# Performance work log

Measured on AMD Instinct MI355X. Metric: run time of the kernel, lower is better.

Reference implementation:

```python
import jax, jax.numpy as jnp
import numpy as np

B, S, H = 2, 2048, 2048
NH, G = 16, 4
HD = H // NH  # 128


def setup_inputs() -> dict:
    key = jax.random.key(0)
    ks = jax.random.split(key, 9)
    sc = 0.02
    x = jax.random.normal(ks[0], (B, S, H), dtype=jnp.float32)
    # causal mask: 1.0 where j > i (masked), added as mask * -1e9 (matches torch code)
    causal_mask = jnp.triu(jnp.ones((S, S), dtype=jnp.float32), k=1)[None, None]
    Wq = jax.random.normal(ks[1], (H, H), dtype=jnp.float32) * sc
    bq = jnp.zeros((H,), dtype=jnp.float32)
    Wk = jax.random.normal(ks[2], (H, G * HD), dtype=jnp.float32) * sc
    bk = jnp.zeros((G * HD,), dtype=jnp.float32)
    Wv = jax.random.normal(ks[3], (H, G * HD), dtype=jnp.float32) * sc
    bv = jnp.zeros((G * HD,), dtype=jnp.float32)
    Wo = jax.random.normal(ks[4], (H, H), dtype=jnp.float32) * sc
    bo = jnp.zeros((H,), dtype=jnp.float32)
    return {"hidden_state": x, "causal_mask": causal_mask,
            "Wq": Wq, "bq": bq, "Wk": Wk, "bk": bk,
            "Wv": Wv, "bv": bv, "Wo": Wo, "bo": bo}


def reference(hidden_state, causal_mask, Wq, bq, Wk, bk, Wv, bv, Wo, bo):
    bsz, seq_len, _ = hidden_state.shape
    npg = NH // G  # query heads per KV group
    q = hidden_state @ Wq + bq                      # [B,S,H]
    k = hidden_state @ Wk + bk                      # [B,S,G*HD]
    v = hidden_state @ Wv + bv                      # [B,S,G*HD]
    # split heads; group query heads by KV group instead of repeating K/V
    q = q.reshape(bsz, seq_len, G, npg, HD).transpose(0, 2, 3, 1, 4)   # [B,G,npg,S,HD]
    k = k.reshape(bsz, seq_len, G, HD).transpose(0, 2, 1, 3)           # [B,G,S,HD]
    v = v.reshape(bsz, seq_len, G, HD).transpose(0, 2, 1, 3)           # [B,G,S,HD]
    scale = 1.0 / jnp.sqrt(jnp.float32(HD))
    scores = jnp.einsum('bgnsd,bgtd->bgnst', q, k) * scale             # [B,G,npg,S,S]
    scores = scores + causal_mask[:, :, None] * (-1e9)
    probs = jax.nn.softmax(scores, axis=-1)
    out = jnp.einsum('bgnst,bgtd->bgnsd', probs, v)                    # [B,G,npg,S,HD]
    out = out.transpose(0, 3, 1, 2, 4).reshape(bsz, seq_len, H)        # [B,S,H]
    return out @ Wo + bo
```

## Files before the change

kernel.cpp:

```cpp
#include <hip/hip_runtime.h>
#include <hip/hip_bf16.h>

#define B_   2
#define S_   2048
#define H_   2048
#define NH_  16
#define G_   4
#define HD_  128
#define NPG_ 4
#define MROWS_ (B_ * S_)
#define KVC_   (G_ * HD_)
#define NT_    (S_ / 64)
#define QSCALE_ 0.08838834764831845f

typedef __attribute__((ext_vector_type(8))) short bf16x8;
typedef __attribute__((ext_vector_type(4))) float f32x4;

__device__ __forceinline__ short f2bf_s(float f) {
    __hip_bfloat16 h = __float2bfloat16(f);
    short s; __builtin_memcpy(&s, &h, 2); return s;
}

__device__ __forceinline__ void gll16(const void* g, void* l) {
    __builtin_amdgcn_global_load_lds(
        (const __attribute__((address_space(1))) unsigned int*)g,
        (__attribute__((address_space(3))) unsigned int*)l, 16, 0, 0);
}

struct alignas(16) bf8pack { short s[8]; };
struct alignas(8)  s4pack  { short s[4]; };

__device__ __forceinline__ bf16x8 ld2x64(const short* p) {
    s4pack lo = *(const s4pack*)p;
    s4pack hi = *(const s4pack*)(p + 4);
    bf16x8 v;
    __builtin_memcpy(&v, &lo, 8);
    __builtin_memcpy((char*)&v + 8, &hi, 8);
    return v;
}

__device__ __forceinline__ void tile_transpose(
    const float* __restrict__ in, __hip_bfloat16* __restrict__ out,
    int R, int C, int bx, int by, int tid) {
    __shared__ short tile[32][33];
    int tx = tid & 31, ty0 = tid >> 5;
    #pragma unroll
    for (int i = 0; i < 32; i += 8)
        tile[ty0 + i][tx] = f2bf_s(in[(size_t)(by * 32 + ty0 + i) * C + bx * 32 + tx]);
    __syncthreads();
    #pragma unroll
    for (int i = 0; i < 32; i += 8) {
        short s = tile[tx][ty0 + i];
        __hip_bfloat16 h; __builtin_memcpy(&h, &s, 2);
        out[(size_t)(bx * 32 + ty0 + i) * R + by * 32 + tx] = h;
    }
}

__global__ __launch_bounds__(256) void prep(
    const float* __restrict__ x,  bf8pack* __restrict__ xb,
    const float* __restrict__ Wq, __hip_bfloat16* __restrict__ WqT,
    const float* __restrict__ Wk, __hip_bfloat16* __restrict__ WkT,
    const float* __restrict__ Wv, __hip_bfloat16* __restrict__ WvT,
    const float* __restrict__ Wo, __hip_bfloat16* __restrict__ WoT,
    const float* __restrict__ bq, const float* __restrict__ bk,
    const float* __restrict__ bv, float* __restrict__ bqkv) {
    const int bid = blockIdx.x, tid = threadIdx.x;
    if (bid < 4096) {
        int i = bid * 256 + tid;
        const float4* p = (const float4*)(x + (size_t)i * 8);
        float4 a = p[0], c = p[1];
        bf8pack o;
        o.s[0] = f2bf_s(a.x); o.s[1] = f2bf_s(a.y);
        o.s[2] = f2bf_s(a.z); o.s[3] = f2bf_s(a.w);
        o.s[4] = f2bf_s(c.x); o.s[5] = f2bf_s(c.y);
        o.s[6] = f2bf_s(c.z); o.s[7] = f2bf_s(c.w);
        xb[i] = o;
    } else if (bid < 8192) {
        int t = bid - 4096;
        tile_transpose(Wq, WqT, H_, H_, t & 63, t >> 6, tid);
    } else if (bid < 9216) {
        int t = bid - 8192;
        tile_transpose(Wk, WkT, H_, KVC_, t & 15, t >> 4, tid);
    } else if (bid < 10240) {
        int t = bid - 9216;
        tile_transpose(Wv, WvT, H_, KVC_, t & 15, t >> 4, tid);
    } else if (bid < 14336) {
        int t = bid - 10240;
        tile_transpose(Wo, WoT, H_, H_, t & 63, t >> 6, tid);
    } else {
        int i = (bid - 14336) * 256 + tid;
        if (i < 3072)
            bqkv[i] = (i < 2048) ? bq[i] : (i < 2560) ? bk[i - 2048] : bv[i - 2560];
    }
}

template <int BM, int NF>
__device__ __forceinline__ void gemm_core(
    const __hip_bfloat16* __restrict__ A,
    const __hip_bfloat16* __restrict__ Bt,
    const int K, const int bm, const int bn,
    short* __restrict__ As, short* __restrict__ Bs,
    f32x4 (* __restrict__ acc)[NF])
{
    constexpr int BN  = 64 * NF;
    constexpr int MH  = BM / 64;
    constexpr int AI  = BM / 64;
    constexpr int ASZ = BM * 64;
    constexpr int BSZ = BN * 64;
    const int t = threadIdx.x;
    const int lane = t & 63, wave = t >> 6;
    const int l15 = lane & 15, quad = lane >> 4;
    const int lrow = lane >> 3, lcg = lane & 7;
    const int wm = (wave >> 2) * (BM / 2);
    const int wn = (wave & 3) * (16 * NF);
    const int nt = K >> 6;

    auto stageA = [&](int ti, int b) {
        const int kt = ti << 6;
        short* Ad = As + b * ASZ;
        #pragma unroll
        for (int p = 0; p < AI; ++p) {
            const int r0 = wave * (AI * 8) + p * 8;
            const int row = r0 + lrow;
            gll16(A + (size_t)(bm + row) * K + kt + ((lcg ^ (row & 7)) << 3),
                  Ad + r0 * 64);
        }
    };
    auto stageB = [&](int ti, int b) {
        const int kt = ti << 6;
        short* Bd = Bs + b * BSZ;
        #pragma unroll
        for (int p = 0; p < NF; ++p) {
            const int r0 = wave * (NF * 8) + p * 8;
            const int row = r0 + lrow;
            gll16(Bt + (size_t)(bn + row) * K + kt + ((lcg ^ (row & 7)) << 3),
                  Bd + r0 * 64);
        }
    };

    stageA(0, 0); stageB(0, 0);
    stageA(1, 1); stageB(1, 1);

    for (int ti = 0; ti < nt; ++ti) {
        const int b = ti & 1;
        const short* Ab = As + b * ASZ;
        const short* Bb = Bs + b * BSZ;

        if (ti == nt - 1) {
            asm volatile("s_waitcnt vmcnt(0)" ::: "memory");
        } else if constexpr (AI + NF == 7) {
            asm volatile("s_waitcnt vmcnt(7)" ::: "memory");
        } else if constexpr (AI + NF == 6) {
            asm volatile("s_waitcnt vmcnt(6)" ::: "memory");
        } else {
            asm volatile("s_waitcnt vmcnt(0)" ::: "memory");
        }
        asm volatile("s_barrier" ::: "memory");

        bf16x8 bfr[NF][2], af0[MH][2], af1[MH][2];
        #pragma unroll
        for (int n = 0; n < NF; ++n) {
            const int rb = wn + n * 16 + l15;
            #pragma unroll
            for (int ks = 0; ks < 2; ++ks)
                bfr[n][ks] = *(const bf16x8*)(Bb + rb * 64 +
                    (((ks * 4 + quad) ^ (rb & 7)) << 3));
        }
        #pragma unroll
        for (int i = 0; i < MH; ++i) {
            const int ra = wm + i * 16 + l15;
            #pragma unroll
            for (int ks = 0; ks < 2; ++ks)
                af0[i][ks] = *(const bf16x8*)(Ab + ra * 64 +
                    (((ks * 4 + quad) ^ (ra & 7)) << 3));
        }
        #pragma unroll
        for (int i = 0; i < MH; ++i) {
            const int ra = wm + (MH + i) * 16 + l15;
            #pragma unroll
            for (int ks = 0; ks < 2; ++ks)
                af1[i][ks] = *(const bf16x8*)(Ab + ra * 64 +
                    (((ks * 4 + quad) ^ (ra & 7)) << 3));
        }

        __builtin_amdgcn_s_setprio(1);
        #pragma unroll
        for (int ks = 0; ks < 2; ++ks)
            #pragma unroll
            for (int i = 0; i < MH; ++i)
                #pragma unroll
                for (int n = 0; n < NF; ++n)
                    acc[i][n] = __builtin_amdgcn_mfma_f32_16x16x32_bf16(
                        af0[i][ks], bfr[n][ks], acc[i][n], 0, 0, 0);
        #pragma unroll
        for (int ks = 0; ks < 2; ++ks)
            #pragma unroll
            for (int i = 0; i < MH; ++i)
                #pragma unroll
                for (int n = 0; n < NF; ++n)
                    acc[MH + i][n] = __builtin_amdgcn_mfma_f32_16x16x32_bf16(
                        af1[i][ks], bfr[n][ks], acc[MH + i][n], 0, 0, 0);
        __builtin_amdgcn_s_setprio(0);

        asm volatile("s_barrier" ::: "memory");
        if (ti + 2 < nt) { stageA(ti + 2, b); stageB(ti + 2, b); }
    }
}

__global__ __launch_bounds__(512, 2) void gemm_qkv8(
    const __hip_bfloat16* __restrict__ A,
    const __hip_bfloat16* __restrict__ Bt,
    const float* __restrict__ bias,
    __hip_bfloat16* __restrict__ Qo,
    __hip_bfloat16* __restrict__ Ko,
    __hip_bfloat16* __restrict__ VtG) {
    __shared__ __align__(16) short As[2 * 256 * 64];
    __shared__ __align__(16) short Bs[2 * 192 * 64];
    const int bid = blockIdx.x;
    const int s = (bid & 7) * 32 + (bid >> 3);
    const int bm = (s & 15) * 256, bn = (s >> 4) * 192;

    f32x4 acc[8][3] = {};
    gemm_core<256, 3>(A, Bt, H_, bm, bn, As, Bs, acc);

    const int t = threadIdx.x;
    const int lane = t & 63, wave = t >> 6;
    const int l15 = lane & 15, quad = lane >> 4;
    const int wm = (wave >> 2) * 128, wn = (wave & 3) * 48;

    #pragma unroll
    for (int i = 0; i < 8; ++i) {
        int row0 = bm + wm + i * 16 + quad * 4;
        #pragma unroll
        for (int j = 0; j < 3; ++j) {
            int c0 = bn + wn + j * 16;
            int colg = c0 + l15;
            float bv = bias[colg];
            if (c0 < 2048) {
                #pragma unroll
                for (int r = 0; r < 4; ++r)
                    Qo[(size_t)(row0 + r) * H_ + colg] =
                        __float2bfloat16((acc[i][j][r] + bv) * QSCALE_);
            } else if (c0 < 2560) {
                #pragma unroll
                for (int r = 0; r < 4; ++r)
                    Ko[(size_t)(row0 + r) * KVC_ + (colg - 2048)] =
                        __float2bfloat16(acc[i][j][r] + bv);
            } else {
                int coll = colg - 2560;
                short s4v[4];
                #pragma unroll
                for (int r = 0; r < 4; ++r) s4v[r] = f2bf_s(acc[i][j][r] + bv);
                *(uint2*)(&VtG[(size_t)coll * MROWS_ + row0]) = *(uint2*)s4v;
            }
        }
    }
}

__global__ __launch_bounds__(512, 2) void gemm_out8(
    const __hip_bfloat16* __restrict__ A,
    const __hip_bfloat16* __restrict__ Bt,
    const float* __restrict__ bias,
    float* __restrict__ C) {
    __shared__ __align__(16) short As[2 * 128 * 64];
    __shared__ __align__(16) short Bs[2 * 256 * 64];
    const int bid = blockIdx.x;
    const int s = (bid & 7) * 32 + (bid >> 3);
    const int bm = (s & 31) * 128, bn = (s >> 5) * 256;

    f32x4 acc[4][4] = {};
    gemm_core<128, 4>(A, Bt, H_, bm, bn, As, Bs, acc);

    const int t = threadIdx.x;
    const int lane = t & 63, wave = t >> 6;
    const int l15 = lane & 15, quad = lane >> 4;
    const int wm = (wave >> 2) * 64, wn = (wave & 3) * 64;

    #pragma unroll
    for (int i = 0; i < 4; ++i) {
        int row0 = bm + wm + i * 16 + quad * 4;
        #pragma unroll
        for (int j = 0; j < 4; ++j) {
            int col = bn + wn + j * 16 + l15;
            float bv = bias[col];
            #pragma unroll
            for (int r = 0; r < 4; ++r)
                C[(size_t)(row0 + r) * H_ + col] = acc[i][j][r] + bv;
        }
    }
}

__global__ __launch_bounds__(256, 2) void attn_causal_gqa(
    const __hip_bfloat16* __restrict__ Q,
    const __hip_bfloat16* __restrict__ K,
    const __hip_bfloat16* __restrict__ VtG,
    __hip_bfloat16* __restrict__ O) {
    __shared__ short KsL[64 * 128];
    __shared__ short VtL[128 * 64];
    __shared__ short Ps[4][2][16 * 72];

    const int h  = blockIdx.x;
    const int b  = h >> 4;
    const int hh = h & 15;
    const int g  = hh >> 2;
    const int qb1 = blockIdx.y;
    const int qb2 = NT_ - 1 - qb1;

    const int t = threadIdx.x;
    const int lane = t & 63, wave = t >> 6;
    const int l15 = lane & 15, quad = lane >> 4;
    const int swz = l15 & 7;

    const __hip_bfloat16* Qb = Q + (size_t)b * S_ * H_ + hh * HD_;
    const __hip_bfloat16* Kb = K + (size_t)b * S_ * KVC_ + g * HD_;
    const __hip_bfloat16* Vg = VtG + (size_t)g * HD_ * MROWS_ + b * S_;

    bf16x8 aq1[4], aq2[4];
    {
        const int qr1 = qb1 * 64 + wave * 16 + l15;
        const int qr2 = qb2 * 64 + wave * 16 + l15;
        #pragma unroll
        for (int kk = 0; kk < 4; ++kk) {
            aq1[kk] = *(const bf16x8*)(Qb + (size_t)qr1 * H_ + kk * 32 + quad * 8);
            aq2[kk] = *(const bf16x8*)(Qb + (size_t)qr2 * H_ + kk * 32 + quad * 8);
        }
    }

    f32x4 o1[8] = {}, o2[8] = {};
    float lp1 = 0.f, lp2 = 0.f;
    const int qrow_loc = wave * 16 + l15;

    for (int tile = 0; tile <= qb2; ++tile) {
        const int key0 = tile * 64;
        const bool do1 = (tile <= qb1);

        #pragma unroll
        for (int p = 0; p < 4; ++p) {
            int R0 = wave * 16 + p * 4;
            int row = R0 + (lane >> 4);
            int cg = ((lane & 15) ^ (row & 7)) * 8;
            gll16(Kb + (size_t)(key0 + row) * KVC_ + cg, &KsL[R0 * 128]);
        }
        #pragma unroll
        for (int p = 0; p < 4; ++p) {
            int R0 = wave * 32 + p * 8;
            int row = R0 + (lane >> 3);
            int cg = ((lane & 7) ^ (row & 7)) * 8;
            gll16(Vg + (size_t)row * MROWS_ + key0 + cg, &VtL[R0 * 64]);
        }
        __syncthreads();

        f32x4 s2[4] = {}, s1[4] = {};
        #pragma unroll
        for (int kk = 0; kk < 4; ++kk) {
            bf16x8 bk[4];
            #pragma unroll
            for (int nt = 0; nt < 4; ++nt)
                bk[nt] = *(const bf16x8*)(
                    &KsL[(nt * 16 + l15) * 128 + (((kk * 4 + quad) ^ swz) * 8)]);
            #pragma unroll
            for (int nt = 0; nt < 4; ++nt)
                s2[nt] = __builtin_amdgcn_mfma_f32_16x16x32_bf16(
                    bk[nt], aq2[kk], s2[nt], 0, 0, 0);
            if (do1) {
                #pragma unroll
                for (int nt = 0; nt < 4; ++nt)
                    s1[nt] = __builtin_amdgcn_mfma_f32_16x16x32_bf16(
                        bk[nt], aq1[kk], s1[nt], 0, 0, 0);
            }
        }

        __asm__ volatile("" ::: "memory");
        short* P2 = &Ps[wave][1][0];
        {
            const bool m2 = (tile == qb2);
            #pragma unroll
            for (int nt = 0; nt < 4; ++nt) {
                s4pack pk;
                #pragma unroll
                for (int r = 0; r < 4; ++r) {
                    float p = __expf(s2[nt][r]);
                    if (m2 && (nt * 16 + quad * 4 + r > qrow_loc)) p = 0.f;
                    lp2 += p;
                    pk.s[r] = f2bf_s(p);
                }
                *(s4pack*)&P2[l15 * 72 + nt * 16 + quad * 4] = pk;
            }
        }
        short* P1 = &Ps[wave][0][0];
        if (do1) {
            const bool m1 = (tile == qb1);
            #pragma unroll
            for (int nt = 0; nt < 4; ++nt) {
                s4pack pk;
                #pragma unroll
                for (int r = 0; r < 4; ++r) {
                    float p = __expf(s1[nt][r]);
                    if (m1 && (nt * 16 + quad * 4 + r > qrow_loc)) p = 0.f;
                    lp1 += p;
                    pk.s[r] = f2bf_s(p);
                }
                *(s4pack*)&P1[l15 * 72 + nt * 16 + quad * 4] = pk;
            }
        }
        __asm__ volatile("" ::: "memory");

        #pragma unroll
        for (int ks = 0; ks < 2; ++ks) {
            bf16x8 ap2 = ld2x64(&P2[l15 * 72 + ks * 32 + quad * 8]);
            bf16x8 ap1;
            if (do1) ap1 = ld2x64(&P1[l15 * 72 + ks * 32 + quad * 8]);
            #pragma unroll
            for (int n2 = 0; n2 < 8; ++n2) {
                bf16x8 bv = *(const bf16x8*)(
                    &VtL[(n2 * 16 + l15) * 64 + (((ks * 4 + quad) ^ swz) * 8)]);
                o2[n2] = __builtin_amdgcn_mfma_f32_16x16x32_bf16(
                    ap2, bv, o2[n2], 0, 0, 0);
                if (do1)
                    o1[n2] = __builtin_amdgcn_mfma_f32_16x16x32_bf16(
                        ap1, bv, o1[n2], 0, 0, 0);
            }
        }
        __syncthreads();
    }

    float L1 = lp1, L2 = lp2;
    L1 += __shfl_xor(L1, 16); L2 += __shfl_xor(L2, 16);
    L1 += __shfl_xor(L1, 32); L2 += __shfl_xor(L2, 32);
    #pragma unroll
    for (int r = 0; r < 4; ++r) {
        float i1 = 1.f / __shfl(L1, quad * 4 + r);
        float i2 = 1.f / __shfl(L2, quad * 4 + r);
        int s1r = qb1 * 64 + wave * 16 + quad * 4 + r;
        int s2r = qb2 * 64 + wave * 16 + quad * 4 + r;
        #pragma unroll
        for (int n2 = 0; n2 < 8; ++n2) {
            int d = n2 * 16 + l15;
            O[((size_t)b * S_ + s1r) * H_ + hh * HD_ + d] = __float2bfloat16(o1[n2][r] * i1);
            O[((size_t)b * S_ + s2r) * H_ + hh * HD_ + d] = __float2bfloat16(o2[n2][r] * i2);
        }
    }
}

extern "C" void kernel_launch(void* const* d_in, const int* in_sizes, int n_in,
                              void* d_out, int out_size, void* d_ws, size_t ws_size,
                              hipStream_t stream) {
    const float* x  = (const float*)d_in[0];
    const float* Wq = (const float*)d_in[2];
    const float* bq = (const float*)d_in[3];
    const float* Wk = (const float*)d_in[4];
    const float* bk = (const float*)d_in[5];
    const float* Wv = (const float*)d_in[6];
    const float* bv = (const float*)d_in[7];
    const float* Wo = (const float*)d_in[8];
    const float* bo = (const float*)d_in[9];
    float* out = (float*)d_out;

    char* ws = (char*)d_ws;
    const size_t MB = 1024 * 1024;
    __hip_bfloat16* xb   = (__hip_bfloat16*)(ws);
    __hip_bfloat16* WT   = (__hip_bfloat16*)(ws + 16 * MB);
    __hip_bfloat16* Kws  = (__hip_bfloat16*)(ws + 28 * MB);
    __hip_bfloat16* VtG  = (__hip_bfloat16*)(ws + 32 * MB);
    __hip_bfloat16* WoT  = (__hip_bfloat16*)(ws + 36 * MB);
    float*          bqkv = (float*)         (ws + 44 * MB);
    __hip_bfloat16* Aws  = (__hip_bfloat16*)(ws);
    __hip_bfloat16* Qbuf = (__hip_bfloat16*)d_out;

    prep<<<14348, 256, 0, stream>>>(
        x, (bf8pack*)xb,
        Wq, WT,
        Wk, WT + (size_t)2048 * H_,
        Wv, WT + (size_t)2560 * H_,
        Wo, WoT,
        bq, bk, bv, bqkv);

    gemm_qkv8<<<256, 512, 0, stream>>>(xb, WT, bqkv, Qbuf, Kws, VtG);

    attn_causal_gqa<<<dim3(B_ * NH_, NT_ / 2), 256, 0, stream>>>(Qbuf, Kws, VtG, Aws);

    gemm_out8<<<256, 512, 0, stream>>>(Aws, WoT, bo, out);
}
```

Baseline: 302.5 us.

## Restructure GEMM core pipelining, widen QKV tiles, and double-buffer K in attention

```diff
diff --git a/kernel.cpp b/kernel.cpp
--- a/kernel.cpp
+++ b/kernel.cpp
@@ -94,30 +94,31 @@
     }
 }
 
-template <int BM, int NF>
+template <int BM>
 __device__ __forceinline__ void gemm_core(
     const __hip_bfloat16* __restrict__ A,
     const __hip_bfloat16* __restrict__ Bt,
     const int K, const int bm, const int bn,
     short* __restrict__ As, short* __restrict__ Bs,
-    f32x4 (* __restrict__ acc)[NF])
+    f32x4 (* __restrict__ acc)[4])
 {
-    constexpr int BN  = 64 * NF;
-    constexpr int MH  = BM / 64;
+    constexpr int MF  = BM / 32;
+    constexpr int MH  = MF / 2;
     constexpr int AI  = BM / 64;
     constexpr int ASZ = BM * 64;
-    constexpr int BSZ = BN * 64;
-    const int t = threadIdx.x;
-    const int lane = t & 63, wave = t >> 6;
+    constexpr int BSZ = 256 * 64;
+    const int t0 = threadIdx.x;
+    const int lane = t0 & 63, wave = t0 >> 6;
     const int l15 = lane & 15, quad = lane >> 4;
     const int lrow = lane >> 3, lcg = lane & 7;
     const int wm = (wave >> 2) * (BM / 2);
-    const int wn = (wave & 3) * (16 * NF);
+    const int wn = (wave & 3) * 64;
     const int nt = K >> 6;
 
-    auto stageA = [&](int ti, int b) {
+    auto stage = [&](int ti) {
         const int kt = ti << 6;
-        short* Ad = As + b * ASZ;
+        short* Ad = As + (ti & 1) * ASZ;
+        short* Bd = Bs + (ti & 1) * BSZ;
         #pragma unroll
         for (int p = 0; p < AI; ++p) {
             const int r0 = wave * (AI * 8) + p * 8;
@@ -125,45 +126,30 @@
             gll16(A + (size_t)(bm + row) * K + kt + ((lcg ^ (row & 7)) << 3),
                   Ad + r0 * 64);
         }
-    };
-    auto stageB = [&](int ti, int b) {
-        const int kt = ti << 6;
-        short* Bd = Bs + b * BSZ;
-        #pragma unroll
-        for (int p = 0; p < NF; ++p) {
-            const int r0 = wave * (NF * 8) + p * 8;
+        #pragma unroll
+        for (int p = 0; p < 4; ++p) {
+            const int r0 = wave * 32 + p * 8;
             const int row = r0 + lrow;
             gll16(Bt + (size_t)(bn + row) * K + kt + ((lcg ^ (row & 7)) << 3),
                   Bd + r0 * 64);
         }
     };
 
-    stageA(0, 0); stageB(0, 0);
-    stageA(1, 1); stageB(1, 1);
-
-    for (int ti = 0; ti < nt; ++ti) {
-        const int b = ti & 1;
-        const short* Ab = As + b * ASZ;
-        const short* Bb = Bs + b * BSZ;
-
-        if (ti == nt - 1) {
-            asm volatile("s_waitcnt vmcnt(0)" ::: "memory");
-        } else if constexpr (AI + NF == 7) {
-            asm volatile("s_waitcnt vmcnt(7)" ::: "memory");
-        } else if constexpr (AI + NF == 6) {
-            asm volatile("s_waitcnt vmcnt(6)" ::: "memory");
-        } else {
-            asm volatile("s_waitcnt vmcnt(0)" ::: "memory");
-        }
-        asm volatile("s_barrier" ::: "memory");
-
-        bf16x8 bfr[NF][2], af0[MH][2], af1[MH][2];
-        #pragma unroll
-        for (int n = 0; n < NF; ++n) {
+    stage(0);
+    asm volatile("s_waitcnt vmcnt(0)" ::: "memory");
+    asm volatile("s_barrier" ::: "memory");
+
+    for (int t = 0; t < nt; ++t) {
+        const short* Ab = As + (t & 1) * ASZ;
+        const short* Bb = Bs + (t & 1) * BSZ;
+        bf16x8 b01[2][2], b23[2][2], ah[MH][2];
+
+        #pragma unroll
+        for (int n = 0; n < 2; ++n) {
             const int rb = wn + n * 16 + l15;
             #pragma unroll
             for (int ks = 0; ks < 2; ++ks)
-                bfr[n][ks] = *(const bf16x8*)(Bb + rb * 64 +
+                b01[n][ks] = *(const bf16x8*)(Bb + rb * 64 +
                     (((ks * 4 + quad) ^ (rb & 7)) << 3));
         }
         #pragma unroll
@@ -171,39 +157,80 @@
             const int ra = wm + i * 16 + l15;
             #pragma unroll
             for (int ks = 0; ks < 2; ++ks)
-                af0[i][ks] = *(const bf16x8*)(Ab + ra * 64 +
+                ah[i][ks] = *(const bf16x8*)(Ab + ra * 64 +
                     (((ks * 4 + quad) ^ (ra & 7)) << 3));
         }
+        if (t + 1 < nt) stage(t + 1);
+        asm volatile("s_barrier" ::: "memory");
+        asm volatile("s_waitcnt lgkmcnt(0)" ::: "memory");
+        __builtin_amdgcn_s_setprio(1);
+        #pragma unroll
+        for (int ks = 0; ks < 2; ++ks)
+            #pragma unroll
+            for (int i = 0; i < MH; ++i)
+                #pragma unroll
+                for (int n = 0; n < 2; ++n)
+                    acc[i][n] = __builtin_amdgcn_mfma_f32_16x16x32_bf16(
+                        ah[i][ks], b01[n][ks], acc[i][n], 0, 0, 0);
+        __builtin_amdgcn_s_setprio(0);
+        asm volatile("s_barrier" ::: "memory");
+
+        #pragma unroll
+        for (int n = 0; n < 2; ++n) {
+            const int rb = wn + (2 + n) * 16 + l15;
+            #pragma unroll
+            for (int ks = 0; ks < 2; ++ks)
+                b23[n][ks] = *(const bf16x8*)(Bb + rb * 64 +
+                    (((ks * 4 + quad) ^ (rb & 7)) << 3));
+        }
+        asm volatile("s_barrier" ::: "memory");
+        asm volatile("s_waitcnt lgkmcnt(0)" ::: "memory");
+        __builtin_amdgcn_s_setprio(1);
+        #pragma unroll
+        for (int ks = 0; ks < 2; ++ks)
+            #pragma unroll
+            for (int i = 0; i < MH; ++i)
+                #pragma unroll
+                for (int n = 0; n < 2; ++n)
+                    acc[i][2 + n] = __builtin_amdgcn_mfma_f32_16x16x32_bf16(
+                        ah[i][ks], b23[n][ks], acc[i][2 + n], 0, 0, 0);
+        __builtin_amdgcn_s_setprio(0);
+        asm volatile("s_barrier" ::: "memory");
+
         #pragma unroll
         for (int i = 0; i < MH; ++i) {
             const int ra = wm + (MH + i) * 16 + l15;
             #pragma unroll
             for (int ks = 0; ks < 2; ++ks)
-                af1[i][ks] = *(const bf16x8*)(Ab + ra * 64 +
+                ah[i][ks] = *(const bf16x8*)(Ab + ra * 64 +
                     (((ks * 4 + quad) ^ (ra & 7)) << 3));
         }
-
+        asm volatile("s_barrier" ::: "memory");
+        asm volatile("s_waitcnt lgkmcnt(0)" ::: "memory");
         __builtin_amdgcn_s_setprio(1);
         #pragma unroll
         for (int ks = 0; ks < 2; ++ks)
             #pragma unroll
             for (int i = 0; i < MH; ++i)
                 #pragma unroll
-                for (int n = 0; n < NF; ++n)
-                    acc[i][n] = __builtin_amdgcn_mfma_f32_16x16x32_bf16(
-                        af0[i][ks], bfr[n][ks], acc[i][n], 0, 0, 0);
+                for (int n = 0; n < 2; ++n)
+                    acc[MH + i][2 + n] = __builtin_amdgcn_mfma_f32_16x16x32_bf16(
+                        ah[i][ks], b23[n][ks], acc[MH + i][2 + n], 0, 0, 0);
+        __builtin_amdgcn_s_setprio(0);
+        asm volatile("s_barrier" ::: "memory");
+
+        __builtin_amdgcn_s_setprio(1);
         #pragma unroll
         for (int ks = 0; ks < 2; ++ks)
             #pragma unroll
             for (int i = 0; i < MH; ++i)
                 #pragma unroll
-                for (int n = 0; n < NF; ++n)
+                for (int n = 0; n < 2; ++n)
                     acc[MH + i][n] = __builtin_amdgcn_mfma_f32_16x16x32_bf16(
-                        af1[i][ks], bfr[n][ks], acc[MH + i][n], 0, 0, 0);
+                        ah[i][ks], b01[n][ks], acc[MH + i][n], 0, 0, 0);
         __builtin_amdgcn_s_setprio(0);
-
-        asm volatile("s_barrier" ::: "memory");
-        if (ti + 2 < nt) { stageA(ti + 2, b); stageB(ti + 2, b); }
+        asm volatile("s_waitcnt vmcnt(0)" ::: "memory");
+        asm volatile("s_barrier" ::: "memory");
     }
 }
 
@@ -215,24 +242,24 @@
     __hip_bfloat16* __restrict__ Ko,
     __hip_bfloat16* __restrict__ VtG) {
     __shared__ __align__(16) short As[2 * 256 * 64];
-    __shared__ __align__(16) short Bs[2 * 192 * 64];
+    __shared__ __align__(16) short Bs[2 * 256 * 64];
     const int bid = blockIdx.x;
-    const int s = (bid & 7) * 32 + (bid >> 3);
-    const int bm = (s & 15) * 256, bn = (s >> 4) * 192;
-
-    f32x4 acc[8][3] = {};
-    gemm_core<256, 3>(A, Bt, H_, bm, bn, As, Bs, acc);
+    const int s = (bid & 7) * 24 + (bid >> 3);
+    const int bm = (s & 15) * 256, bn = (s >> 4) * 256;
+
+    f32x4 acc[8][4] = {};
+    gemm_core<256>(A, Bt, H_, bm, bn, As, Bs, acc);
 
     const int t = threadIdx.x;
     const int lane = t & 63, wave = t >> 6;
     const int l15 = lane & 15, quad = lane >> 4;
-    const int wm = (wave >> 2) * 128, wn = (wave & 3) * 48;
+    const int wm = (wave >> 2) * 128, wn = (wave & 3) * 64;
 
     #pragma unroll
     for (int i = 0; i < 8; ++i) {
         int row0 = bm + wm + i * 16 + quad * 4;
         #pragma unroll
-        for (int j = 0; j < 3; ++j) {
+        for (int j = 0; j < 4; ++j) {
             int c0 = bn + wn + j * 16;
             int colg = c0 + l15;
             float bv = bias[colg];
@@ -269,7 +296,7 @@
     const int bm = (s & 31) * 128, bn = (s >> 5) * 256;
 
     f32x4 acc[4][4] = {};
-    gemm_core<128, 4>(A, Bt, H_, bm, bn, As, Bs, acc);
+    gemm_core<128>(A, Bt, H_, bm, bn, As, Bs, acc);
 
     const int t = threadIdx.x;
     const int lane = t & 63, wave = t >> 6;
@@ -295,9 +322,9 @@
     const __hip_bfloat16* __restrict__ K,
     const __hip_bfloat16* __restrict__ VtG,
     __hip_bfloat16* __restrict__ O) {
-    __shared__ short KsL[64 * 128];
+    __shared__ short KsL[2][64 * 128];
     __shared__ short VtL[128 * 64];
-    __shared__ short Ps[4][2][16 * 72];
+    __shared__ short Ps[4][2][16 * 76];
 
     const int h  = blockIdx.x;
     const int b  = h >> 4;
@@ -315,6 +342,26 @@
     const __hip_bfloat16* Kb = K + (size_t)b * S_ * KVC_ + g * HD_;
     const __hip_bfloat16* Vg = VtG + (size_t)g * HD_ * MROWS_ + b * S_;
 
+    auto stageK = [&](int tile) {
+        short* kd = &KsL[tile & 1][0];
+        #pragma unroll
+        for (int p = 0; p < 4; ++p) {
+            int R0 = wave * 16 + p * 4;
+            int row = R0 + (lane >> 4);
+            int cg = ((lane & 15) ^ (row & 7)) * 8;
+            gll16(Kb + (size_t)(tile * 64 + row) * KVC_ + cg, &kd[R0 * 128]);
+        }
+    };
+    auto stageV = [&](int tile) {
+        #pragma unroll
+        for (int p = 0; p < 4; ++p) {
+            int R0 = wave * 32 + p * 8;
+            int row = R0 + (lane >> 3);
+            int cg = ((lane & 7) ^ (row & 7)) * 8;
+            gll16(Vg + (size_t)row * MROWS_ + tile * 64 + cg, &VtL[R0 * 64]);
+        }
+    };
+
     bf16x8 aq1[4], aq2[4];
     {
         const int qr1 = qb1 * 64 + wave * 16 + l15;
@@ -330,25 +377,20 @@
     float lp1 = 0.f, lp2 = 0.f;
     const int qrow_loc = wave * 16 + l15;
 
+    stageK(0);
+
     for (int tile = 0; tile <= qb2; ++tile) {
-        const int key0 = tile * 64;
         const bool do1 = (tile <= qb1);
-
-        #pragma unroll
-        for (int p = 0; p < 4; ++p) {
-            int R0 = wave * 16 + p * 4;
-            int row = R0 + (lane >> 4);
-            int cg = ((lane & 15) ^ (row & 7)) * 8;
-            gll16(Kb + (size_t)(key0 + row) * KVC_ + cg, &KsL[R0 * 128]);
-        }
-        #pragma unroll
-        for (int p = 0; p < 4; ++p) {
-            int R0 = wave * 32 + p * 8;
-            int row = R0 + (lane >> 3);
-            int cg = ((lane & 7) ^ (row & 7)) * 8;
-            gll16(Vg + (size_t)row * MROWS_ + key0 + cg, &VtL[R0 * 64]);
-        }
-        __syncthreads();
+        const bool last = (tile == qb2);
+
+        stageV(tile);
+        if (!last) stageK(tile + 1);
+
+        if (!last) asm volatile("s_waitcnt vmcnt(8)" ::: "memory");
+        else       asm volatile("s_waitcnt vmcnt(4)" ::: "memory");
+        asm volatile("s_barrier" ::: "memory");
+
+        const short* kb = &KsL[tile & 1][0];
 
         f32x4 s2[4] = {}, s1[4] = {};
         #pragma unroll
@@ -357,7 +399,7 @@
             #pragma unroll
             for (int nt = 0; nt < 4; ++nt)
                 bk[nt] = *(const bf16x8*)(
-                    &KsL[(nt * 16 + l15) * 128 + (((kk * 4 + quad) ^ swz) * 8)]);
+                    &kb[(nt * 16 + l15) * 128 + (((kk * 4 + quad) ^ swz) * 8)]);
             #pragma unroll
             for (int nt = 0; nt < 4; ++nt)
                 s2[nt] = __builtin_amdgcn_mfma_f32_16x16x32_bf16(
@@ -384,7 +426,7 @@
                     lp2 += p;
                     pk.s[r] = f2bf_s(p);
                 }
-                *(s4pack*)&P2[l15 * 72 + nt * 16 + quad * 4] = pk;
+                *(s4pack*)&P2[l15 * 76 + nt * 16 + quad * 4] = pk;
             }
         }
         short* P1 = &Ps[wave][0][0];
@@ -400,16 +442,20 @@
                     lp1 += p;
                     pk.s[r] = f2bf_s(p);
                 }
-                *(s4pack*)&P1[l15 * 72 + nt * 16 + quad * 4] = pk;
+                *(s4pack*)&P1[l15 * 76 + nt * 16 + quad * 4] = pk;
             }
         }
         __asm__ volatile("" ::: "memory");
 
+        if (!last) asm volatile("s_waitcnt vmcnt(4)" ::: "memory");
+        else       asm volatile("s_waitcnt vmcnt(0)" ::: "memory");
+        asm volatile("s_barrier" ::: "memory");
+
         #pragma unroll
         for (int ks = 0; ks < 2; ++ks) {
-            bf16x8 ap2 = ld2x64(&P2[l15 * 72 + ks * 32 + quad * 8]);
+            bf16x8 ap2 = ld2x64(&P2[l15 * 76 + ks * 32 + quad * 8]);
             bf16x8 ap1;
-            if (do1) ap1 = ld2x64(&P1[l15 * 72 + ks * 32 + quad * 8]);
+            if (do1) ap1 = ld2x64(&P1[l15 * 76 + ks * 32 + quad * 8]);
             #pragma unroll
             for (int n2 = 0; n2 < 8; ++n2) {
                 bf16x8 bv = *(const bf16x8*)(
@@ -421,7 +467,7 @@
                         ap1, bv, o1[n2], 0, 0, 0);
             }
         }
-        __syncthreads();
+        asm volatile("s_barrier" ::: "memory");
     }
 
     float L1 = lp1, L2 = lp2;
@@ -475,7 +521,7 @@
         Wo, WoT,
         bq, bk, bv, bqkv);
 
-    gemm_qkv8<<<256, 512, 0, stream>>>(xb, WT, bqkv, Qbuf, Kws, VtG);
+    gemm_qkv8<<<192, 512, 0, stream>>>(xb, WT, bqkv, Qbuf, Kws, VtG);
 
     attn_causal_gqa<<<dim3(B_ * NH_, NT_ / 2), 256, 0, stream>>>(Qbuf, Kws, VtG, Aws);
 
```

New measurement: 311.7 us. 3.1% more time.
